# Kernel tuning notes

Measured on AMD Instinct MI355X. Metric: run time of the kernel, lower is better.

The kernel has to match this reference:

```python
import jax, jax.numpy as jnp
import numpy as np

B, S, D, H, DFF = 2, 2048, 512, 8, 2048
DK = D // H
EPS = 1e-6  # LayerNormalization eps


def _ln(x, a, b):
    # torch: alpha * (x - mean) / (std + eps) + bias, std is unbiased (ddof=1)
    m = jnp.mean(x, axis=-1, keepdims=True)
    s = jnp.std(x, axis=-1, keepdims=True, ddof=1)
    return a * (x - m) / (s + EPS) + b


def _mha(Q, K, V, mask, Wq, bq, Wk, bk, Wv, bv, Wo, bo):
    Bq, Sq = Q.shape[0], Q.shape[1]
    Sk = K.shape[1]
    q = (Q @ Wq + bq).reshape(Bq, Sq, H, DK).transpose(0, 2, 1, 3)  # bhqd
    k = (K @ Wk + bk).reshape(Bq, Sk, H, DK).transpose(0, 2, 1, 3)  # bhkd
    v = (V @ Wv + bv).reshape(Bq, Sk, H, DK).transpose(0, 2, 1, 3)  # bhkd
    scores = jnp.einsum('bhqd,bhkd->bhqk', q, k) / jnp.sqrt(jnp.float32(DK))
    scores = jnp.where(mask == 0, -jnp.inf, scores)  # masked_fill(mask==0, -inf)
    attn = jax.nn.softmax(scores, axis=-1)  # dropout is identity in eval
    out = jnp.einsum('bhqk,bhkd->bhqd', attn, v)
    out = out.transpose(0, 2, 1, 3).reshape(Bq, Sq, D)
    return out @ Wo + bo


def setup_inputs() -> dict:
    key = jax.random.key(0)
    ks = jax.random.split(key, 20)
    sc = 0.02
    inp = {
        'x': jax.random.normal(ks[0], (B, S, D), jnp.float32),
        'encoder_output': jax.random.normal(ks[1], (B, S, D), jnp.float32),
        'encoder_output_mask': jnp.broadcast_to(jnp.ones((S, S), jnp.int32), (B, 1, S, S)),
        'decoder_mask': jnp.broadcast_to(jnp.tril(jnp.ones((S, S), jnp.int32)), (B, 1, S, S)),
        'sa_Wq': jax.random.normal(ks[2], (D, D), jnp.float32) * sc,
        'sa_bq': jnp.zeros((D,), jnp.float32),
        'sa_Wk': jax.random.normal(ks[3], (D, D), jnp.float32) * sc,
        'sa_bk': jnp.zeros((D,), jnp.float32),
        'sa_Wv': jax.random.normal(ks[4], (D, D), jnp.float32) * sc,
        'sa_bv': jnp.zeros((D,), jnp.float32),
        'sa_Wo': jax.random.normal(ks[5], (D, D), jnp.float32) * sc,
        'sa_bo': jnp.zeros((D,), jnp.float32),
        'ca_Wq': jax.random.normal(ks[6], (D, D), jnp.float32) * sc,
        'ca_bq': jnp.zeros((D,), jnp.float32),
        'ca_Wk': jax.random.normal(ks[7], (D, D), jnp.float32) * sc,
        'ca_bk': jnp.zeros((D,), jnp.float32),
        'ca_Wv': jax.random.normal(ks[8], (D, D), jnp.float32) * sc,
        'ca_bv': jnp.zeros((D,), jnp.float32),
        'ca_Wo': jax.random.normal(ks[9], (D, D), jnp.float32) * sc,
        'ca_bo': jnp.zeros((D,), jnp.float32),
        'ff_W1': jax.random.normal(ks[10], (D, DFF), jnp.float32) * sc,
        'ff_b1': jnp.zeros((DFF,), jnp.float32),
        'ff_W2': jax.random.normal(ks[11], (DFF, D), jnp.float32) * sc,
        'ff_b2': jnp.zeros((D,), jnp.float32),
        'ln0_a': jnp.ones((1,), jnp.float32), 'ln0_b': jnp.zeros((1,), jnp.float32),
        'ln1_a': jnp.ones((1,), jnp.float32), 'ln1_b': jnp.zeros((1,), jnp.float32),
        'ln2_a': jnp.ones((1,), jnp.float32), 'ln2_b': jnp.zeros((1,), jnp.float32),
    }
    return inp


def reference(x, encoder_output, encoder_output_mask, decoder_mask,
              sa_Wq, sa_bq, sa_Wk, sa_bk, sa_Wv, sa_bv, sa_Wo, sa_bo,
              ca_Wq, ca_bq, ca_Wk, ca_bk, ca_Wv, ca_bv, ca_Wo, ca_bo,
              ff_W1, ff_b1, ff_W2, ff_b2,
              ln0_a, ln0_b, ln1_a, ln1_b, ln2_a, ln2_b):
    # Residual 0: pre-norm self-attention (dropout = identity in eval)
    n = _ln(x, ln0_a, ln0_b)
    x = x + _mha(n, n, n, decoder_mask, sa_Wq, sa_bq, sa_Wk, sa_bk, sa_Wv, sa_bv, sa_Wo, sa_bo)
    # Residual 1: pre-norm cross-attention
    n = _ln(x, ln1_a, ln1_b)
    x = x + _mha(n, encoder_output, encoder_output, encoder_output_mask,
                 ca_Wq, ca_bq, ca_Wk, ca_bk, ca_Wv, ca_bv, ca_Wo, ca_bo)
    # Residual 2: pre-norm FFN (Linear -> ReLU -> Linear)
    n = _ln(x, ln2_a, ln2_b)
    x = x + (jax.nn.relu(n @ ff_W1 + ff_b1) @ ff_W2 + ff_b2)
    return x
```

## Files before the change

kernel.cpp:

```cpp
#include <hip/hip_runtime.h>
#include <hip/hip_bf16.h>

typedef __bf16 bf16_t;
typedef _Float16 f16_t;
typedef __bf16 bf16x8_t __attribute__((ext_vector_type(8)));
typedef _Float16 f16x4_t __attribute__((ext_vector_type(4)));
typedef float f32x4_t __attribute__((ext_vector_type(4)));

static constexpr int B_ = 2, S_ = 2048, D_ = 512, H_ = 8, DK_ = 64, DFF_ = 2048;
static constexpr int M_ = B_ * S_;
static constexpr float QSCALE = 0.125f * 1.44269504f;

#if __has_builtin(__builtin_amdgcn_mfma_f32_16x16x16_f16)
#define MFMA16F16 __builtin_amdgcn_mfma_f32_16x16x16_f16
#else
#define MFMA16F16 __builtin_amdgcn_mfma_f32_16x16x16f16
#endif

__device__ __forceinline__ unsigned pkbf(float a, float b) {
  union { bf16_t h; unsigned short u; } x, y;
  x.h = (bf16_t)a; y.h = (bf16_t)b;
  return (unsigned)x.u | ((unsigned)y.u << 16);
}

__device__ __forceinline__ void async16(void* lds, const void* g) {
  __builtin_amdgcn_global_load_lds((const __attribute__((address_space(1))) void*)g,
                                   (__attribute__((address_space(3))) void*)lds,
                                   16, 0, 0);
}

struct PrepArg {
  const float* W[10]; bf16_t* T[10];
  const float* enc; bf16_t* encb;
  const float* x; bf16_t* xb; float2* stats0;
  float* stats12;
  float* csum[7];
};

__global__ __launch_bounds__(256) void prep(PrepArg a) {
  __shared__ float T[64 * 65];
  const int bx = blockIdx.x, tid = threadIdx.x;
  if (bx < 1024) {
    const float* W; bf16_t* Wt; int K, N, k0, n0;
    if (bx < 512) { int wi = bx >> 6, t = bx & 63; W = a.W[wi]; Wt = a.T[wi]; K = 512; N = 512; k0 = (t >> 3) * 64; n0 = (t & 7) * 64; }
    else if (bx < 768) { int t = bx - 512; W = a.W[8]; Wt = a.T[8]; K = 512; N = 2048; k0 = (t & 7) * 64; n0 = (t >> 3) * 64; }
    else { int t = bx - 768; W = a.W[9]; Wt = a.T[9]; K = 2048; N = 512; k0 = (t & 31) * 64; n0 = (t >> 5) * 64; }
#pragma unroll
    for (int p = 0; p < 4; ++p) {
      int e = p * 1024 + tid * 4;
      int kr = e >> 6, nc = e & 63;
      float4 f = *(const float4*)(W + (long)(k0 + kr) * N + n0 + nc);
      T[kr * 65 + nc + 0] = f.x; T[kr * 65 + nc + 1] = f.y;
      T[kr * 65 + nc + 2] = f.z; T[kr * 65 + nc + 3] = f.w;
    }
    __syncthreads();
#pragma unroll
    for (int p = 0; p < 2; ++p) {
      int e = p * 2048 + tid * 8;
      int nr = e >> 6, kc = e & 63;
      alignas(16) bf16_t t8[8];
#pragma unroll
      for (int j = 0; j < 8; ++j) t8[j] = (bf16_t)T[(kc + j) * 65 + nr];
      *(uint4*)(Wt + (long)(n0 + nr) * K + k0 + kc) = *(uint4*)t8;
    }
  } else if (bx < 2048) {
    const long i = ((long)(bx - 1024) * 256 + tid) * 8;
    float4 u = *(const float4*)(a.enc + i);
    float4 v = *(const float4*)(a.enc + i + 4);
    alignas(16) bf16_t t[8];
    t[0] = (bf16_t)u.x; t[1] = (bf16_t)u.y; t[2] = (bf16_t)u.z; t[3] = (bf16_t)u.w;
    t[4] = (bf16_t)v.x; t[5] = (bf16_t)v.y; t[6] = (bf16_t)v.z; t[7] = (bf16_t)v.w;
    *(uint4*)(a.encb + i) = *(uint4*)t;
  } else if (bx < 3072) {
    const int row = (bx - 2048) * 4 + (tid >> 6);
    const int lane = tid & 63;
    const float4* xr = (const float4*)(a.x + (long)row * D_);
    float4 v0 = xr[lane * 2], v1 = xr[lane * 2 + 1];
    float s = v0.x + v0.y + v0.z + v0.w + v1.x + v1.y + v1.z + v1.w;
    float ss = v0.x * v0.x + v0.y * v0.y + v0.z * v0.z + v0.w * v0.w +
               v1.x * v1.x + v1.y * v1.y + v1.z * v1.z + v1.w * v1.w;
#pragma unroll
    for (int m = 1; m < 64; m <<= 1) { s += __shfl_xor(s, m); ss += __shfl_xor(ss, m); }
    alignas(16) bf16_t y[8];
    y[0] = (bf16_t)v0.x; y[1] = (bf16_t)v0.y; y[2] = (bf16_t)v0.z; y[3] = (bf16_t)v0.w;
    y[4] = (bf16_t)v1.x; y[5] = (bf16_t)v1.y; y[6] = (bf16_t)v1.z; y[7] = (bf16_t)v1.w;
    ((uint4*)(a.xb + (long)row * D_))[lane] = *(uint4*)y;
    if (lane == 0) a.stats0[row] = make_float2(s, ss);
  } else if (bx < 3079) {
    const int wsel = bx - 3072;
    const int map[6] = {0, 1, 2, 4, 5, 6};
    const float* Wsrc = (wsel < 6) ? a.W[map[wsel]] : a.W[8];
    float* dst = a.csum[wsel];
    if (wsel < 6) {
      float ax = 0.f, ay = 0.f;
      const float2* p = (const float2*)Wsrc + tid;
      for (int k = 0; k < 512; ++k) { float2 v = p[(long)k * 256]; ax += v.x; ay += v.y; }
      ((float2*)dst)[tid] = make_float2(ax, ay);
    } else {
      float acc[8] = {0, 0, 0, 0, 0, 0, 0, 0};
      for (int k = 0; k < 512; ++k) {
        float4 u = *(const float4*)(Wsrc + (long)k * 2048 + tid * 8);
        float4 v = *(const float4*)(Wsrc + (long)k * 2048 + tid * 8 + 4);
        acc[0] += u.x; acc[1] += u.y; acc[2] += u.z; acc[3] += u.w;
        acc[4] += v.x; acc[5] += v.y; acc[6] += v.z; acc[7] += v.w;
      }
      *(float4*)(dst + tid * 8) = make_float4(acc[0], acc[1], acc[2], acc[3]);
      *(float4*)(dst + tid * 8 + 4) = make_float4(acc[4], acc[5], acc[6], acc[7]);
    }
  } else {
    const int i = (bx - 3079) * 2048 + tid * 8;
    *(f32x4_t*)&a.stats12[i] = (f32x4_t){0.f, 0.f, 0.f, 0.f};
    *(f32x4_t*)&a.stats12[i + 4] = (f32x4_t){0.f, 0.f, 0.f, 0.f};
  }
}

__device__ __forceinline__ void ln_coef(float2 st, float ga, float gb,
                                        float& sc, float& sh) {
  const float mean = st.x * (1.0f / 512.0f);
  float var = (st.y - 512.0f * mean * mean) * (1.0f / 511.0f);
  var = fmaxf(var, 0.0f);
  sc = ga / (sqrtf(var) + 1e-6f);
  sh = gb - mean * sc;
}

struct GQ {
  const bf16_t* A[3]; const bf16_t* Wt[3];
  const float* bias[3]; const float* csum[3];
  void* out[3]; float osc[3];
  const float2* stats; const float* ga; const float* gb;
  int N; int zvt;
};

template <int RELU>
__global__ __launch_bounds__(256, 4) void gemmQ(GQ a) {
  __shared__ bf16_t As[2][64 * 64];
  __shared__ bf16_t Bs[2][64 * 64];
  const int z = blockIdx.z;
  const bf16_t* A = a.A[z];
  const bf16_t* Wt = a.Wt[z];
  const float* bias = a.bias[z];
  const float* csum = a.csum[z];
  const int N = a.N;
  const int tid = threadIdx.x;
  const int wave = tid >> 6, lane = tid & 63, quad = lane >> 4, l15 = lane & 15;
  const long m0 = (long)blockIdx.x * 64;
  const long n0 = (long)blockIdx.y * 64;
  const int wm = (wave >> 1) * 32;
  const int wn = (wave & 1) * 32;

  const int r8 = lane >> 3;
  const int cg = (lane & 7) ^ r8;
  const bf16_t* Ab = A + m0 * 512 + cg * 8;
  const bf16_t* Bb = Wt + n0 * 512 + cg * 8;

  auto stage = [&](int buf, int k0) {
#pragma unroll
    for (int c = 0; c < 2; ++c) {
      const int row = wave * 16 + c * 8;
      async16(&As[buf][row * 64], Ab + (long)(row + r8) * 512 + k0);
      async16(&Bs[buf][row * 64], Bb + (long)(row + r8) * 512 + k0);
    }
  };

  f32x4_t acc[2][2];
#pragma unroll
  for (int i = 0; i < 2; ++i)
#pragma unroll
    for (int j = 0; j < 2; ++j) acc[i][j] = (f32x4_t){0.f, 0.f, 0.f, 0.f};

  stage(0, 0);
  for (int kt = 0; kt < 8; ++kt) {
    __syncthreads();
    if (kt + 1 < 8) stage((kt + 1) & 1, (kt + 1) * 64);
    const bf16_t* Al = &As[kt & 1][0];
    const bf16_t* Bl = &Bs[kt & 1][0];
#pragma unroll
    for (int ks = 0; ks < 2; ++ks) {
      const int sc = ((ks * 4 + quad) ^ (l15 & 7)) * 8;
      bf16x8_t af[2], bfr[2];
#pragma unroll
      for (int i = 0; i < 2; ++i) {
        af[i] = *(const bf16x8_t*)&Al[(wm + i * 16 + l15) * 64 + sc];
        bfr[i] = *(const bf16x8_t*)&Bl[(wn + i * 16 + l15) * 64 + sc];
      }
#pragma unroll
      for (int i = 0; i < 2; ++i)
#pragma unroll
        for (int j = 0; j < 2; ++j)
          acc[i][j] = __builtin_amdgcn_mfma_f32_16x16x32_bf16(af[i], bfr[j], acc[i][j], 0, 0, 0);
    }
  }

  const bool useln = (csum != nullptr);
  float scr[2][4], shr[2][4];
  if (useln) {
    const float gav = a.ga[0], gbv = a.gb[0];
#pragma unroll
    for (int i = 0; i < 2; ++i)
#pragma unroll
      for (int r = 0; r < 4; ++r) {
        const int row = (int)m0 + wm + i * 16 + quad * 4 + r;
        ln_coef(a.stats[row], gav, gbv, scr[i][r], shr[i][r]);
      }
  } else {
#pragma unroll
    for (int i = 0; i < 2; ++i)
#pragma unroll
      for (int r = 0; r < 4; ++r) { scr[i][r] = 1.f; shr[i][r] = 0.f; }
  }

  const bool isVt = (z == a.zvt);
  const float osc = a.osc[z];
#pragma unroll
  for (int i = 0; i < 2; ++i) {
#pragma unroll
    for (int j = 0; j < 2; ++j) {
      const int col = (int)n0 + wn + j * 16 + l15;
      const float cs = useln ? csum[col] : 0.f;
      const float bv = bias[col];
      float v[4];
#pragma unroll
      for (int r = 0; r < 4; ++r) {
        v[r] = scr[i][r] * acc[i][j][r] + shr[i][r] * cs + bv;
        if constexpr (RELU == 1) v[r] = fmaxf(v[r], 0.f);
      }
      if (isVt) {
        const int row0 = (int)m0 + wm + i * 16 + quad * 4;
        const int b = row0 >> 11, s = row0 & 2047;
        const long addr = ((long)(b * 8 + (col >> 6)) * 64 + (col & 63)) * 2048 + s;
        union { f16_t h[4]; uint2 u; } w;
#pragma unroll
        for (int r = 0; r < 4; ++r) w.h[r] = (f16_t)v[r];
        *(uint2*)((f16_t*)a.out[z] + addr) = w.u;
      } else {
        bf16_t* outp = (bf16_t*)a.out[z];
#pragma unroll
        for (int r = 0; r < 4; ++r) {
          const long row = m0 + wm + i * 16 + quad * 4 + r;
          outp[row * N + col] = (bf16_t)(v[r] * osc);
        }
      }
    }
  }
}

template <bool STATS>
__global__ __launch_bounds__(256, 4) void gemmR(const bf16_t* __restrict__ A, int K,
                                                const bf16_t* __restrict__ Wt,
                                                const float* __restrict__ bias,
                                                const float* __restrict__ res,
                                                float* __restrict__ out,
                                                bf16_t* __restrict__ outb,
                                                float* __restrict__ statsOut) {
  __shared__ bf16_t As[2][64 * 64];
  __shared__ bf16_t Bs[2][64 * 64];
  const int tid = threadIdx.x;
  const int wave = tid >> 6, lane = tid & 63, quad = lane >> 4, l15 = lane & 15;
  const long m0 = (long)blockIdx.x * 64;
  const long n0 = (long)blockIdx.y * 64;
  const int wm = (wave >> 1) * 32;
  const int wn = (wave & 1) * 32;

  const int r8 = lane >> 3;
  const int cg = (lane & 7) ^ r8;
  const bf16_t* Ab = A + m0 * (long)K + cg * 8;
  const bf16_t* Bb = Wt + n0 * (long)K + cg * 8;

  auto stage = [&](int buf, int k0) {
#pragma unroll
    for (int c = 0; c < 2; ++c) {
      const int row = wave * 16 + c * 8;
      async16(&As[buf][row * 64], Ab + (long)(row + r8) * K + k0);
      async16(&Bs[buf][row * 64], Bb + (long)(row + r8) * K + k0);
    }
  };

  f32x4_t acc[2][2];
#pragma unroll
  for (int i = 0; i < 2; ++i)
#pragma unroll
    for (int j = 0; j < 2; ++j) acc[i][j] = (f32x4_t){0.f, 0.f, 0.f, 0.f};

  const int KT = K >> 6;
  stage(0, 0);
  for (int kt = 0; kt < KT; ++kt) {
    __syncthreads();
    if (kt + 1 < KT) stage((kt + 1) & 1, (kt + 1) * 64);
    const bf16_t* Al = &As[kt & 1][0];
    const bf16_t* Bl = &Bs[kt & 1][0];
#pragma unroll
    for (int ks = 0; ks < 2; ++ks) {
      const int sc = ((ks * 4 + quad) ^ (l15 & 7)) * 8;
      bf16x8_t af[2], bfr[2];
#pragma unroll
      for (int i = 0; i < 2; ++i) {
        af[i] = *(const bf16x8_t*)&Al[(wm + i * 16 + l15) * 64 + sc];
        bfr[i] = *(const bf16x8_t*)&Bl[(wn + i * 16 + l15) * 64 + sc];
      }
#pragma unroll
      for (int i = 0; i < 2; ++i)
#pragma unroll
        for (int j = 0; j < 2; ++j)
          acc[i][j] = __builtin_amdgcn_mfma_f32_16x16x32_bf16(af[i], bfr[j], acc[i][j], 0, 0, 0);
    }
  }

#pragma unroll
  for (int i = 0; i < 2; ++i) {
    float rs[4] = {0.f, 0.f, 0.f, 0.f}, rq[4] = {0.f, 0.f, 0.f, 0.f};
#pragma unroll
    for (int j = 0; j < 2; ++j) {
      const int col = (int)n0 + wn + j * 16 + l15;
      const float bv = bias[col];
#pragma unroll
      for (int r = 0; r < 4; ++r) {
        const long row = m0 + wm + i * 16 + quad * 4 + r;
        const float v = acc[i][j][r] + bv + res[row * 512 + col];
        out[row * 512 + col] = v;
        if constexpr (STATS) {
          outb[row * 512 + col] = (bf16_t)v;
          rs[r] += v;
          rq[r] += v * v;
        }
      }
    }
    if constexpr (STATS) {
#pragma unroll
      for (int r = 0; r < 4; ++r) {
#pragma unroll
        for (int m = 1; m < 16; m <<= 1) {
          rs[r] += __shfl_xor(rs[r], m);
          rq[r] += __shfl_xor(rq[r], m);
        }
        if (l15 == 0) {
          const long row = m0 + wm + i * 16 + quad * 4 + r;
          atomicAdd(&statsOut[row * 2], rs[r]);
          atomicAdd(&statsOut[row * 2 + 1], rq[r]);
        }
      }
    }
  }
}

template <bool CAUSAL>
__global__ __launch_bounds__(256, 4) void flash_attn(const bf16_t* __restrict__ Q,
                                                     const bf16_t* __restrict__ Kg,
                                                     const f16_t* __restrict__ Vt,
                                                     float* __restrict__ po,
                                                     float* __restrict__ pl) {
  __shared__ bf16_t Ks[2][64 * 64];
  __shared__ f16_t Vs[2][64 * 64];
  const int tid = threadIdx.x, wave = tid >> 6, lane = tid & 63;
  const int quad = lane >> 4, l15 = lane & 15;
  const int bh = blockIdx.y, b = bh >> 3, h = bh & 7;
  const int qt = CAUSAL ? (15 - (int)blockIdx.x) : (int)blockIdx.x;
  const int chunk = blockIdx.z;
  const int ntt = CAUSAL ? (2 * qt + 2) : 32;
  const int tstart = (chunk * ntt) / 3;
  const int tend = ((chunk + 1) * ntt) / 3;
  const int q0 = qt * 128;
  const long prow0 = ((long)(chunk * 16 + bh)) * 2048;

  if (tstart >= tend) {
    const long ob = (prow0 + q0) * 64;
#pragma unroll
    for (int p = 0; p < 8; ++p)
      *(f32x4_t*)&po[ob + (long)tid * 32 + p * 4] = (f32x4_t){0.f, 0.f, 0.f, 0.f};
    if (tid < 128) pl[prow0 + q0 + tid] = 0.f;
    return;
  }

  const int qw = q0 + wave * 32;
  const long base = (long)b * S_ * D_ + (long)h * DK_;
  const long vtbase = (long)bh * DK_ * S_;

  bf16x8_t qf[2][2];
#pragma unroll
  for (int qh = 0; qh < 2; ++qh)
#pragma unroll
    for (int ks = 0; ks < 2; ++ks)
      qf[qh][ks] = *(const bf16x8_t*)(Q + base + (long)(qw + qh * 16 + l15) * D_ + ks * 32 + quad * 8);

  const int r8 = lane >> 3;
  const int cg8 = (lane & 7) ^ r8;
  const bf16_t* Kb = Kg + base + cg8 * 8;
  const f16_t* Vb = Vt + vtbase + cg8 * 8;

  auto stage = [&](int buf, int t) {
    const int kk0 = t * 64;
#pragma unroll
    for (int c = 0; c < 2; ++c) {
      const int row = wave * 16 + c * 8;
      async16(&Ks[buf][row * 64], Kb + (long)(kk0 + row + r8) * D_);
      async16(&Vs[buf][row * 64], Vb + (long)(row + r8) * S_ + kk0);
    }
  };

  float li[2] = {0.f, 0.f};
  f32x4_t o[2][4];
#pragma unroll
  for (int qh = 0; qh < 2; ++qh)
#pragma unroll
    for (int db = 0; db < 4; ++db) o[qh][db] = (f32x4_t){0.f, 0.f, 0.f, 0.f};

  stage(0, tstart);
  for (int t = tstart; t < tend; ++t) {
    const int buf = (t - tstart) & 1;
    __syncthreads();
    if (t + 1 < tend) stage(buf ^ 1, t + 1);
    const bf16_t* Kt = &Ks[buf][0];
    const f16_t* Vl = &Vs[buf][0];
    const int kk0 = t * 64;

    f16x4_t pa[2][4];
#pragma unroll
    for (int qh = 0; qh < 2; ++qh) {
      f32x4_t st[4];
#pragma unroll
      for (int nb = 0; nb < 4; ++nb) {
        f32x4_t acc = (f32x4_t){0.f, 0.f, 0.f, 0.f};
#pragma unroll
        for (int ks = 0; ks < 2; ++ks) {
          const int scf = ((ks * 4 + quad) ^ (l15 & 7)) * 8;
          const bf16x8_t kf = *(const bf16x8_t*)&Kt[(nb * 16 + l15) * 64 + scf];
          acc = __builtin_amdgcn_mfma_f32_16x16x32_bf16(kf, qf[qh][ks], acc, 0, 0, 0);
        }
        st[nb] = acc;
      }
      const bool domask = CAUSAL && (kk0 + 63 > qw + qh * 16);
#pragma unroll
      for (int nb = 0; nb < 4; ++nb) {
#pragma unroll
        for (int r = 0; r < 4; ++r) {
          float v = st[nb][r];
          if (domask && (kk0 + nb * 16 + quad * 4 + r > qw + qh * 16 + l15)) v = -1e30f;
          const float p = exp2f(v);
          st[nb][r] = p;
          li[qh] += p;
        }
        pa[qh][nb] = (f16x4_t){(f16_t)st[nb][0], (f16_t)st[nb][1],
                               (f16_t)st[nb][2], (f16_t)st[nb][3]};
      }
    }

#pragma unroll
    for (int k4 = 0; k4 < 4; ++k4) {
#pragma unroll
      for (int db = 0; db < 4; ++db) {
        const int row = db * 16 + l15;
        const int c = 2 * k4 + (quad >> 1);
        const f16x4_t vf = *(const f16x4_t*)&Vl[row * 64 + ((c ^ (l15 & 7)) * 8) + (quad & 1) * 4];
#pragma unroll
        for (int qh = 0; qh < 2; ++qh)
          o[qh][db] = MFMA16F16(vf, pa[qh][k4], o[qh][db], 0, 0, 0);
      }
    }
  }

#pragma unroll
  for (int qh = 0; qh < 2; ++qh) {
    li[qh] += __shfl_xor(li[qh], 16);
    li[qh] += __shfl_xor(li[qh], 32);
    const long pr = prow0 + qw + qh * 16 + l15;
#pragma unroll
    for (int db = 0; db < 4; ++db)
      *(f32x4_t*)&po[pr * 64 + db * 16 + quad * 4] = o[qh][db];
    if (quad == 0) pl[pr] = li[qh];
  }
}

__global__ __launch_bounds__(256) void merge3(const float* __restrict__ po,
                                              const float* __restrict__ pl,
                                              bf16_t* __restrict__ O) {
  const int qt = blockIdx.x, bh = blockIdx.y, b = bh >> 3, h = bh & 7;
  const int t = threadIdx.x;
  const int q = qt * 64 + (t >> 2), d0 = (t & 3) * 16;
  const long r0 = (long)bh * 2048 + q;
  const long r1 = (long)(16 + bh) * 2048 + q;
  const long r2 = (long)(32 + bh) * 2048 + q;
  const float inv = 1.0f / (pl[r0] + pl[r1] + pl[r2]);
  alignas(16) bf16_t out[16];
#pragma unroll
  for (int j = 0; j < 4; ++j) {
    f32x4_t x0 = *(const f32x4_t*)&po[r0 * 64 + d0 + j * 4];
    f32x4_t x1 = *(const f32x4_t*)&po[r1 * 64 + d0 + j * 4];
    f32x4_t x2 = *(const f32x4_t*)&po[r2 * 64 + d0 + j * 4];
#pragma unroll
    for (int r = 0; r < 4; ++r) out[j * 4 + r] = (bf16_t)((x0[r] + x1[r] + x2[r]) * inv);
  }
  const long row = (long)b * S_ + q;
  *(uint4*)(O + row * D_ + h * DK_ + d0) = *(uint4*)&out[0];
  *(uint4*)(O + row * D_ + h * DK_ + d0 + 8) = *(uint4*)&out[8];
}

extern "C" void kernel_launch(void* const* d_in, const int* in_sizes, int n_in,
                              void* d_out, int out_size, void* d_ws, size_t ws_size,
                              hipStream_t stream) {
  const float* x    = (const float*)d_in[0];
  const float* enc  = (const float*)d_in[1];
  const float* saWq = (const float*)d_in[4];  const float* sabq = (const float*)d_in[5];
  const float* saWk = (const float*)d_in[6];  const float* sabk = (const float*)d_in[7];
  const float* saWv = (const float*)d_in[8];  const float* sabv = (const float*)d_in[9];
  const float* saWo = (const float*)d_in[10]; const float* sabo = (const float*)d_in[11];
  const float* caWq = (const float*)d_in[12]; const float* cabq = (const float*)d_in[13];
  const float* caWk = (const float*)d_in[14]; const float* cabk = (const float*)d_in[15];
  const float* caWv = (const float*)d_in[16]; const float* cabv = (const float*)d_in[17];
  const float* caWo = (const float*)d_in[18]; const float* cabo = (const float*)d_in[19];
  const float* ffW1 = (const float*)d_in[20]; const float* ffb1 = (const float*)d_in[21];
  const float* ffW2 = (const float*)d_in[22]; const float* ffb2 = (const float*)d_in[23];
  const float* ln0a = (const float*)d_in[24]; const float* ln0b = (const float*)d_in[25];
  const float* ln1a = (const float*)d_in[26]; const float* ln1b = (const float*)d_in[27];
  const float* ln2a = (const float*)d_in[28]; const float* ln2b = (const float*)d_in[29];

  char* ws = (char*)d_ws;
  size_t off = 0;
  auto alloc = [&](size_t bytes) -> void* {
    void* p = ws + off;
    off += (bytes + 255) & ~(size_t)255;
    return p;
  };
  bf16_t* wt_saq = (bf16_t*)alloc(512 * 512 * 2);
  bf16_t* wt_sak = (bf16_t*)alloc(512 * 512 * 2);
  bf16_t* wt_sav = (bf16_t*)alloc(512 * 512 * 2);
  bf16_t* wt_sao = (bf16_t*)alloc(512 * 512 * 2);
  bf16_t* wt_caq = (bf16_t*)alloc(512 * 512 * 2);
  bf16_t* wt_cak = (bf16_t*)alloc(512 * 512 * 2);
  bf16_t* wt_cav = (bf16_t*)alloc(512 * 512 * 2);
  bf16_t* wt_cao = (bf16_t*)alloc(512 * 512 * 2);
  bf16_t* wt_f1  = (bf16_t*)alloc((size_t)512 * 2048 * 2);
  bf16_t* wt_f2  = (bf16_t*)alloc((size_t)2048 * 512 * 2);
  bf16_t* enc_b  = (bf16_t*)alloc((size_t)M_ * D_ * 2);
  bf16_t* xb     = (bf16_t*)alloc((size_t)M_ * D_ * 2);
  bf16_t* qb     = (bf16_t*)alloc((size_t)M_ * D_ * 2);
  bf16_t* kb     = (bf16_t*)alloc((size_t)M_ * D_ * 2);
  f16_t*  vtb    = (f16_t*)alloc((size_t)M_ * D_ * 2);
  bf16_t* attnb  = (bf16_t*)alloc((size_t)M_ * D_ * 2);
  bf16_t* hid    = (bf16_t*)alloc((size_t)M_ * DFF_ * 2);
  float*  x2     = (float*)alloc((size_t)M_ * D_ * 4);
  float*  x1     = (float*)alloc((size_t)M_ * D_ * 4);
  bf16_t* x1b    = (bf16_t*)alloc((size_t)M_ * D_ * 2);
  bf16_t* x2b    = (bf16_t*)alloc((size_t)M_ * D_ * 2);
  float*  pl     = (float*)alloc(3 * 16 * 2048 * 4);
  float2* stats0 = (float2*)alloc(4096 * 8);
  float*  stats12= (float*)alloc(2 * 4096 * 2 * 4);
  float*  cs_saq = (float*)alloc(512 * 4);
  float*  cs_sak = (float*)alloc(512 * 4);
  float*  cs_sav = (float*)alloc(512 * 4);
  float*  cs_caq = (float*)alloc(512 * 4);
  float*  cs_cak = (float*)alloc(512 * 4);
  float*  cs_cav = (float*)alloc(512 * 4);
  float*  cs_f1  = (float*)alloc(2048 * 4);
  float*  po     = (float*)hid;
  float*  stats1 = stats12;
  float*  stats2 = stats12 + 8192;

  {
    PrepArg a;
    a.W[0] = saWq; a.T[0] = wt_saq; a.W[1] = saWk; a.T[1] = wt_sak;
    a.W[2] = saWv; a.T[2] = wt_sav; a.W[3] = saWo; a.T[3] = wt_sao;
    a.W[4] = caWq; a.T[4] = wt_caq; a.W[5] = caWk; a.T[5] = wt_cak;
    a.W[6] = caWv; a.T[6] = wt_cav; a.W[7] = caWo; a.T[7] = wt_cao;
    a.W[8] = ffW1; a.T[8] = wt_f1;  a.W[9] = ffW2; a.T[9] = wt_f2;
    a.enc = enc; a.encb = enc_b; a.x = x; a.xb = xb; a.stats0 = stats0;
    a.stats12 = stats12;
    a.csum[0] = cs_saq; a.csum[1] = cs_sak; a.csum[2] = cs_sav;
    a.csum[3] = cs_caq; a.csum[4] = cs_cak; a.csum[5] = cs_cav;
    a.csum[6] = cs_f1;
    prep<<<3087, 256, 0, stream>>>(a);
  }

  {
    GQ g;
    g.A[0] = xb; g.A[1] = xb; g.A[2] = xb;
    g.Wt[0] = wt_saq; g.Wt[1] = wt_sak; g.Wt[2] = wt_sav;
    g.bias[0] = sabq; g.bias[1] = sabk; g.bias[2] = sabv;
    g.csum[0] = cs_saq; g.csum[1] = cs_sak; g.csum[2] = cs_sav;
    g.out[0] = qb; g.out[1] = kb; g.out[2] = vtb;
    g.osc[0] = QSCALE; g.osc[1] = 1.f; g.osc[2] = 1.f;
    g.stats = stats0; g.ga = ln0a; g.gb = ln0b; g.N = 512; g.zvt = 2;
    gemmQ<0><<<dim3(64, 8, 3), 256, 0, stream>>>(g);
  }
  flash_attn<true><<<dim3(16, 16, 3), 256, 0, stream>>>(qb, kb, vtb, po, pl);
  merge3<<<dim3(32, 16), 256, 0, stream>>>(po, pl, attnb);
  gemmR<true><<<dim3(64, 8), 256, 0, stream>>>(attnb, 512, wt_sao, sabo, x, x1, x1b, stats1);

  {
    GQ g;
    g.A[0] = x1b; g.A[1] = enc_b; g.A[2] = enc_b;
    g.Wt[0] = wt_caq; g.Wt[1] = wt_cak; g.Wt[2] = wt_cav;
    g.bias[0] = cabq; g.bias[1] = cabk; g.bias[2] = cabv;
    g.csum[0] = cs_caq; g.csum[1] = nullptr; g.csum[2] = nullptr;
    g.out[0] = qb; g.out[1] = kb; g.out[2] = vtb;
    g.osc[0] = QSCALE; g.osc[1] = 1.f; g.osc[2] = 1.f;
    g.stats = (const float2*)stats1; g.ga = ln1a; g.gb = ln1b; g.N = 512; g.zvt = 2;
    gemmQ<0><<<dim3(64, 8, 3), 256, 0, stream>>>(g);
  }
  flash_attn<false><<<dim3(16, 16, 3), 256, 0, stream>>>(qb, kb, vtb, po, pl);
  merge3<<<dim3(32, 16), 256, 0, stream>>>(po, pl, attnb);
  gemmR<true><<<dim3(64, 8), 256, 0, stream>>>(attnb, 512, wt_cao, cabo, x1, x2, x2b, stats2);

  {
    GQ g;
    g.A[0] = x2b; g.Wt[0] = wt_f1; g.bias[0] = ffb1; g.csum[0] = cs_f1;
    g.out[0] = hid; g.osc[0] = 1.f;
    g.A[1] = x2b; g.Wt[1] = wt_f1; g.bias[1] = ffb1; g.csum[1] = cs_f1;
    g.out[1] = hid; g.osc[1] = 1.f;
    g.A[2] = x2b; g.Wt[2] = wt_f1; g.bias[2] = ffb1; g.csum[2] = cs_f1;
    g.out[2] = hid; g.osc[2] = 1.f;
    g.stats = (const float2*)stats2; g.ga = ln2a; g.gb = ln2b; g.N = 2048; g.zvt = -1;
    gemmQ<1><<<dim3(64, 32, 1), 256, 0, stream>>>(g);
  }
  gemmR<false><<<dim3(64, 8), 256, 0, stream>>>(hid, 2048, wt_f2, ffb2, x2, (float*)d_out, nullptr, nullptr);
}
```

Baseline: 398.0 us.

## Split weight column-sum reductions across blocks with atomics and stage V-transpose via LDS

The column-sum reductions in prep previously ran on only 7 blocks, each looping over all 512 rows, which made them a serial tail. They now split the K dimension across 96 + 32 blocks and combine partial sums with float atomicAdd into a buffer zeroed by a hipMemsetAsync. That memset also replaces the stats12 zeroing blocks. Separately, the V-transpose output in the QKV GEMM is staged through LDS so each thread writes 32-byte contiguous chunks instead of scattered 8-byte stores. The costs are an extra memset launch, atomic contention, and non-deterministic summation order.

```diff
diff --git a/kernel.cpp b/kernel.cpp
--- a/kernel.cpp
+++ b/kernel.cpp
@@ -33,7 +33,6 @@
   const float* W[10]; bf16_t* T[10];
   const float* enc; bf16_t* encb;
   const float* x; bf16_t* xb; float2* stats0;
-  float* stats12;
   float* csum[7];
 };
 
@@ -86,31 +85,33 @@
     y[4] = (bf16_t)v1.x; y[5] = (bf16_t)v1.y; y[6] = (bf16_t)v1.z; y[7] = (bf16_t)v1.w;
     ((uint4*)(a.xb + (long)row * D_))[lane] = *(uint4*)y;
     if (lane == 0) a.stats0[row] = make_float2(s, ss);
-  } else if (bx < 3079) {
-    const int wsel = bx - 3072;
+  } else if (bx < 3168) {
+    const int b3 = bx - 3072;
     const int map[6] = {0, 1, 2, 4, 5, 6};
-    const float* Wsrc = (wsel < 6) ? a.W[map[wsel]] : a.W[8];
+    const int wsel = b3 >> 4;
+    const int k0r = (b3 & 15) * 32;
+    const float* Wsrc = a.W[map[wsel]];
     float* dst = a.csum[wsel];
-    if (wsel < 6) {
-      float ax = 0.f, ay = 0.f;
-      const float2* p = (const float2*)Wsrc + tid;
-      for (int k = 0; k < 512; ++k) { float2 v = p[(long)k * 256]; ax += v.x; ay += v.y; }
-      ((float2*)dst)[tid] = make_float2(ax, ay);
-    } else {
-      float acc[8] = {0, 0, 0, 0, 0, 0, 0, 0};
-      for (int k = 0; k < 512; ++k) {
-        float4 u = *(const float4*)(Wsrc + (long)k * 2048 + tid * 8);
-        float4 v = *(const float4*)(Wsrc + (long)k * 2048 + tid * 8 + 4);
-        acc[0] += u.x; acc[1] += u.y; acc[2] += u.z; acc[3] += u.w;
-        acc[4] += v.x; acc[5] += v.y; acc[6] += v.z; acc[7] += v.w;
-      }
-      *(float4*)(dst + tid * 8) = make_float4(acc[0], acc[1], acc[2], acc[3]);
-      *(float4*)(dst + tid * 8 + 4) = make_float4(acc[4], acc[5], acc[6], acc[7]);
-    }
+    float ax = 0.f, ay = 0.f;
+    const float2* p = (const float2*)Wsrc + (long)k0r * 256 + tid;
+#pragma unroll 4
+    for (int k = 0; k < 32; ++k) { float2 v = p[(long)k * 256]; ax += v.x; ay += v.y; }
+    atomicAdd(&dst[2 * tid], ax);
+    atomicAdd(&dst[2 * tid + 1], ay);
   } else {
-    const int i = (bx - 3079) * 2048 + tid * 8;
-    *(f32x4_t*)&a.stats12[i] = (f32x4_t){0.f, 0.f, 0.f, 0.f};
-    *(f32x4_t*)&a.stats12[i + 4] = (f32x4_t){0.f, 0.f, 0.f, 0.f};
+    const int k0r = (bx - 3168) * 16;
+    const float* Wsrc = a.W[8];
+    float* dst = a.csum[6];
+    float acc[8] = {0, 0, 0, 0, 0, 0, 0, 0};
+#pragma unroll 2
+    for (int k = 0; k < 16; ++k) {
+      float4 u = *(const float4*)(Wsrc + (long)(k0r + k) * 2048 + tid * 8);
+      float4 v = *(const float4*)(Wsrc + (long)(k0r + k) * 2048 + tid * 8 + 4);
+      acc[0] += u.x; acc[1] += u.y; acc[2] += u.z; acc[3] += u.w;
+      acc[4] += v.x; acc[5] += v.y; acc[6] += v.z; acc[7] += v.w;
+    }
+#pragma unroll
+    for (int j = 0; j < 8; ++j) atomicAdd(&dst[tid * 8 + j], acc[j]);
   }
 }
 
@@ -211,6 +212,9 @@
 
   const bool isVt = (z == a.zvt);
   const float osc = a.osc[z];
+  f16_t* Tp = (f16_t*)&As[0][0];
+  if (isVt) __syncthreads();
+
 #pragma unroll
   for (int i = 0; i < 2; ++i) {
 #pragma unroll
@@ -225,13 +229,10 @@
         if constexpr (RELU == 1) v[r] = fmaxf(v[r], 0.f);
       }
       if (isVt) {
-        const int row0 = (int)m0 + wm + i * 16 + quad * 4;
-        const int b = row0 >> 11, s = row0 & 2047;
-        const long addr = ((long)(b * 8 + (col >> 6)) * 64 + (col & 63)) * 2048 + s;
-        union { f16_t h[4]; uint2 u; } w;
-#pragma unroll
-        for (int r = 0; r < 4; ++r) w.h[r] = (f16_t)v[r];
-        *(uint2*)((f16_t*)a.out[z] + addr) = w.u;
+        const int dl = wn + j * 16 + l15;
+        const int sl = wm + i * 16 + quad * 4;
+#pragma unroll
+        for (int r = 0; r < 4; ++r) Tp[dl * 72 + sl + r] = (f16_t)v[r];
       } else {
         bf16_t* outp = (bf16_t*)a.out[z];
 #pragma unroll
@@ -241,6 +242,20 @@
         }
       }
     }
+  }
+
+  if (isVt) {
+    __syncthreads();
+    const int dl = tid >> 2, sc4 = (tid & 3) * 16;
+    alignas(16) f16_t t16[16];
+#pragma unroll
+    for (int j = 0; j < 16; ++j) t16[j] = Tp[dl * 72 + sc4 + j];
+    const int b = (int)(m0 >> 11), sbase = (int)(m0 & 2047);
+    const int dg = (int)n0 + dl;
+    const int h = dg >> 6, dih = dg & 63;
+    f16_t* dstp = (f16_t*)a.out[z] + ((long)(b * 8 + h) * 64 + dih) * 2048 + sbase + sc4;
+    *(uint4*)dstp = *(uint4*)&t16[0];
+    *(uint4*)(dstp + 8) = *(uint4*)&t16[8];
   }
 }
 
@@ -542,17 +557,19 @@
   bf16_t* x2b    = (bf16_t*)alloc((size_t)M_ * D_ * 2);
   float*  pl     = (float*)alloc(3 * 16 * 2048 * 4);
   float2* stats0 = (float2*)alloc(4096 * 8);
-  float*  stats12= (float*)alloc(2 * 4096 * 2 * 4);
-  float*  cs_saq = (float*)alloc(512 * 4);
-  float*  cs_sak = (float*)alloc(512 * 4);
-  float*  cs_sav = (float*)alloc(512 * 4);
-  float*  cs_caq = (float*)alloc(512 * 4);
-  float*  cs_cak = (float*)alloc(512 * 4);
-  float*  cs_cav = (float*)alloc(512 * 4);
-  float*  cs_f1  = (float*)alloc(2048 * 4);
+  float*  zr     = (float*)alloc((5120 + 16384) * 4);
+  float*  cs_saq = zr + 0;
+  float*  cs_sak = zr + 512;
+  float*  cs_sav = zr + 1024;
+  float*  cs_caq = zr + 1536;
+  float*  cs_cak = zr + 2048;
+  float*  cs_cav = zr + 2560;
+  float*  cs_f1  = zr + 3072;
+  float*  stats1 = zr + 5120;
+  float*  stats2 = zr + 13312;
   float*  po     = (float*)hid;
-  float*  stats1 = stats12;
-  float*  stats2 = stats12 + 8192;
+
+  hipMemsetAsync(zr, 0, (5120 + 16384) * 4, stream);
 
   {
     PrepArg a;
@@ -562,11 +579,10 @@
     a.W[6] = caWv; a.T[6] = wt_cav; a.W[7] = caWo; a.T[7] = wt_cao;
     a.W[8] = ffW1; a.T[8] = wt_f1;  a.W[9] = ffW2; a.T[9] = wt_f2;
     a.enc = enc; a.encb = enc_b; a.x = x; a.xb = xb; a.stats0 = stats0;
-    a.stats12 = stats12;
     a.csum[0] = cs_saq; a.csum[1] = cs_sak; a.csum[2] = cs_sav;
     a.csum[3] = cs_caq; a.csum[4] = cs_cak; a.csum[5] = cs_cav;
     a.csum[6] = cs_f1;
-    prep<<<3087, 256, 0, stream>>>(a);
+    prep<<<3200, 256, 0, stream>>>(a);
   }
 
   {
```

Result: faster. 360.0 us (-9.5%).
